# Kernel tuning notes

Hardware: AMD Instinct MI355X
Metric: run time of the kernel (lower is better)

Reference implementation:

```python
import jax, jax.numpy as jnp
import numpy as np

IN, H, T = 512, 1024, 1024


def _xavier(key, shape):
    a = (6.0 / (shape[0] + shape[1])) ** 0.5
    return jax.random.uniform(key, shape, minval=-a, maxval=a, dtype=jnp.float32)


def setup_inputs() -> dict:
    key = jax.random.key(0)
    ks = jax.random.split(key, 20)
    inp = {
        'x': jax.random.normal(ks[0], (1, T, IN), dtype=jnp.float32),
        'time': jax.random.uniform(ks[1], (T,), dtype=jnp.float32),
    }
    # initial states ~ N(0, 0.1) as in the source forward
    names = ['h0_1', 'c0_1', 'h0_2', 'c0_2', 'h0_3', 'c0_3']
    for i, n in enumerate(names):
        inp[n] = 0.1 * jax.random.normal(ks[2 + i], (1, H), dtype=jnp.float32)
    # LSTMCell params: weights xavier_uniform, biases uniform(0,1) (torch gate order i,f,g,o)
    inp['W_ih1'] = _xavier(ks[8], (4 * H, IN + 1))
    inp['W_hh1'] = _xavier(ks[9], (4 * H, H))
    inp['b_ih1'] = jax.random.uniform(ks[10], (4 * H,), dtype=jnp.float32)
    inp['b_hh1'] = jax.random.uniform(ks[11], (4 * H,), dtype=jnp.float32)
    inp['W_ih2'] = _xavier(ks[12], (4 * H, H))
    inp['W_hh2'] = _xavier(ks[13], (4 * H, H))
    inp['b_ih2'] = jax.random.uniform(ks[14], (4 * H,), dtype=jnp.float32)
    inp['b_hh2'] = jax.random.uniform(ks[15], (4 * H,), dtype=jnp.float32)
    return inp


def reference(x, time, h0_1, c0_1, h0_2, c0_2, h0_3, c0_3,
              W_ih1, W_hh1, b_ih1, b_hh1, W_ih2, W_hh2, b_ih2, b_hh2):
    def cell(xt, h, c, W_ih, W_hh, b_ih, b_hh):
        gates = xt @ W_ih.T + b_ih + h @ W_hh.T + b_hh  # (1, 4H)
        i, f, g, o = jnp.split(gates, 4, axis=-1)
        c_new = jax.nn.sigmoid(f) * c + jax.nn.sigmoid(i) * jnp.tanh(g)
        h_new = jax.nn.sigmoid(o) * jnp.tanh(c_new)
        return h_new, c_new

    xs = jnp.concatenate([x[0], time[:, None]], axis=1)  # (T, IN+1)

    def step(carry, xt):
        h1, c1, h2, c2, h3, c3 = carry
        h1, c1 = cell(xt[None, :], h1, c1, W_ih1, W_hh1, b_ih1, b_hh1)
        h2, c2 = cell(h1, h2, c2, W_ih2, W_hh2, b_ih2, b_hh2)
        # source calls self.lstm2 again for the third layer (lstm3 unused)
        h3, c3 = cell(h2, h3, c3, W_ih2, W_hh2, b_ih2, b_hh2)
        return (h1, c1, h2, c2, h3, c3), h3[0]

    carry, hs = jax.lax.scan(step, (h0_1, c0_1, h0_2, c0_2, h0_3, c0_3), xs)
    hs = hs[None]              # (1, T, H)
    h_final = carry[4]         # (1, H) -- last h3
    attn = jnp.einsum('bth,bh->bt', hs, h_final)
    w = jax.nn.softmax(attn, axis=1)
    context = jnp.einsum('bth,bt->bh', hs, w)  # (1, H)
    return context
```

## Files before the change

### kernel.cpp

```cpp
#include <hip/hip_runtime.h>
#include <hip/hip_fp16.h>

#define TSTEPS 1024
#define HDIM   1024
#define INDIM  512
#define NGATE  4096
#define NWG_L1  64
#define NWG_L23 128
#define NWG_TOT 192
#define POISON_U 0x7C7C7C7Cu
#define SPIN_MAX (1 << 20)


typedef _Float16 half2v __attribute__((ext_vector_type(2)));
typedef decltype(__builtin_amdgcn_cvt_pkrtz(0.f, 0.f)) f16x2b;

#define PINU(v) asm volatile("" : "+v"(v))

#if defined(__has_builtin)
#if __has_builtin(__builtin_amdgcn_fdot2)
#define HAVE_FDOT2 1
#endif
#endif

#ifdef HAVE_FDOT2
__device__ __forceinline__ float dot2f(unsigned h, unsigned w, float c) {
    return __builtin_amdgcn_fdot2(__builtin_bit_cast(f16x2b, h),
                                  __builtin_bit_cast(f16x2b, w), c, false);
}
#else
__device__ __forceinline__ float dot2f(unsigned h, unsigned w, float c) {
    half2v a = __builtin_bit_cast(half2v, h);
    half2v b = __builtin_bit_cast(half2v, w);
    c = fmaf((float)a[0], (float)b[0], c);
    c = fmaf((float)a[1], (float)b[1], c);
    return c;
}
#endif

__device__ __forceinline__ float wave_sum64_dpp(float v) {
    int x;
    x = __builtin_amdgcn_update_dpp(0, __float_as_int(v), 0x111, 0xf, 0xf, false); v += __int_as_float(x);
    x = __builtin_amdgcn_update_dpp(0, __float_as_int(v), 0x112, 0xf, 0xf, false); v += __int_as_float(x);
    x = __builtin_amdgcn_update_dpp(0, __float_as_int(v), 0x114, 0xf, 0xf, false); v += __int_as_float(x);
    x = __builtin_amdgcn_update_dpp(0, __float_as_int(v), 0x118, 0xf, 0xf, false); v += __int_as_float(x);
    x = __builtin_amdgcn_update_dpp(0, __float_as_int(v), 0x142, 0xa, 0xf, false); v += __int_as_float(x);
    x = __builtin_amdgcn_update_dpp(0, __float_as_int(v), 0x143, 0xc, 0xf, false); v += __int_as_float(x);
    return v;
}

__device__ __forceinline__ float sigm(float x) { return 1.f / (1.f + __expf(-x)); }
__device__ __forceinline__ float fast_tanh(float x) {
    float t = __expf(-2.f * fabsf(x));
    float r = (1.f - t) / (1.f + t);
    return copysignf(r, x);
}

__device__ __forceinline__ unsigned pack_h(float a, float b) {
    auto p = __builtin_amdgcn_cvt_pkrtz(a, b);
    return __builtin_bit_cast(unsigned, p);
}

__device__ __forceinline__ unsigned agent_loadu(const unsigned* p) {
    return __hip_atomic_load(const_cast<unsigned*>(p), __ATOMIC_RELAXED,
                             __HIP_MEMORY_SCOPE_AGENT);
}
__device__ __forceinline__ void agent_storeu(unsigned* p, unsigned v) {
    __hip_atomic_store(p, v, __ATOMIC_RELAXED, __HIP_MEMORY_SCOPE_AGENT);
}
__device__ __forceinline__ float agent_loadf(const float* p) {
    return __hip_atomic_load(const_cast<float*>(p), __ATOMIC_RELAXED,
                             __HIP_MEMORY_SCOPE_AGENT);
}
__device__ __forceinline__ void agent_storef(float* p, float v) {
    __hip_atomic_store(p, v, __ATOMIC_RELAXED, __HIP_MEMORY_SCOPE_AGENT);
}
__device__ __forceinline__ bool isp(float v) { return __float_as_uint(v) == POISON_U; }

__global__ __launch_bounds__(256) void pack_f16(
    const float* __restrict__ src, unsigned* __restrict__ dst, int n)
{
    int i = blockIdx.x * 256 + threadIdx.x;
    if (i < n) {
        float2 v = *(const float2*)(src + 2 * (size_t)i);
        dst[i] = (unsigned)__half_as_ushort(__float2half(v.x)) |
                 ((unsigned)__half_as_ushort(__float2half(v.y)) << 16);
    }
}

#define BM 64
#define BN 64
#define BK 32
#define GK (INDIM + 1)

__device__ __forceinline__ void gemm_tile(
    int bm, int bn, int ttid,
    const float* __restrict__ B, const float* __restrict__ bias1,
    const float* __restrict__ bias2, float* C,
    const float* __restrict__ x, const float* __restrict__ timev,
    float (*As)[BM + 4], float (*Bs)[BN + 4])
{
    const int t0 = bm * BM;
    const int n0 = bn * BN;
    const int tx = ttid & 15;
    const int ty = ttid >> 4;

    float acc[4][4] = {{0.f}};

    for (int kc = 0; kc < GK; kc += BK) {
#pragma unroll
        for (int i = 0; i < 8; i++) {
            int idx = ttid + i * 256;
            int r = idx >> 5;
            int c = idx & 31;
            int col = kc + c;
            int trow = t0 + r;
            float av = (col < INDIM) ? x[(size_t)trow * INDIM + col]
                                     : ((col == INDIM) ? timev[trow] : 0.f);
            As[c][r] = av;
            int nrow = n0 + r;
            Bs[c][r] = (col < GK) ? B[(size_t)nrow * GK + col] : 0.f;
        }
        __syncthreads();

#pragma unroll
        for (int kk = 0; kk < BK; kk++) {
            float a[4], b[4];
#pragma unroll
            for (int i = 0; i < 4; i++) a[i] = As[kk][ty * 4 + i];
#pragma unroll
            for (int j = 0; j < 4; j++) b[j] = Bs[kk][tx * 4 + j];
#pragma unroll
            for (int i = 0; i < 4; i++)
#pragma unroll
                for (int j = 0; j < 4; j++)
                    acc[i][j] = fmaf(a[i], b[j], acc[i][j]);
        }
        __syncthreads();
    }

#pragma unroll
    for (int i = 0; i < 4; i++) {
        int trow = t0 + ty * 4 + i;
#pragma unroll
        for (int j = 0; j < 4; j++) {
            int n = n0 + tx * 4 + j;
            agent_storef(C + (size_t)trow * NGATE + n,
                         acc[i][j] + bias1[n] + bias2[n]);
        }
    }
}

__global__ __launch_bounds__(1024, 4) void fused_scan(
    const unsigned* __restrict__ Wp1,
    float* G1,
    const unsigned* __restrict__ Wpi2,
    const unsigned* __restrict__ Wph2,
    const float* __restrict__ Wih1,
    const float* __restrict__ bih1, const float* __restrict__ bhh1,
    const float* __restrict__ xin, const float* __restrict__ timev,
    const float* bih2, const float* bhh2,
    const float* h0_1, const float* c0_1,
    const float* h0_2, const float* c0_2,
    const float* h0_3, const float* c0_3,
    unsigned* H1p, unsigned* H2p, unsigned* H3p,
    float* H3f)
{
    __shared__ unsigned shp1[512];
    __shared__ unsigned shp2[512];
    __shared__ unsigned shp3[512];
    __shared__ float gbuf[16][4];
    __shared__ float AsT[4][BK][BM + 4];
    __shared__ float BsT[4][BK][BN + 4];

    const int tid = threadIdx.x;
    const int wg  = blockIdx.x;
    const int q   = tid >> 6;
    const int s   = tid & 63;

    if (wg < NWG_L1) {
        const int u0 = wg << 4;
        const int u  = u0 + q;
        unsigned w[4][8];
#pragma unroll
        for (int g = 0; g < 4; ++g) {
            const unsigned* row = Wp1 + (size_t)((g << 10) + u) * 512 + s;
#pragma unroll
            for (int m = 0; m < 8; ++m)
                w[g][m] = row[64 * m];
        }
        float c1 = (tid < 16) ? c0_1[u0 + tid] : 0.f;
        unsigned pv = 0u;

        for (int t = 0; t < TSTEPS; ++t) {
#pragma unroll
            for (int g = 0; g < 4; ++g)
#pragma unroll
                for (int m = 0; m < 8; ++m) PINU(w[g][m]);

            float Gv0 = 0.f, Gv1 = 0.f, Gv2 = 0.f, Gv3 = 0.f;
            if (tid < 16) {
                const float* gptr = G1 + (size_t)t * NGATE + u0 + tid;
                Gv0 = agent_loadf(gptr);
                Gv1 = agent_loadf(gptr + 1024);
                Gv2 = agent_loadf(gptr + 2048);
                Gv3 = agent_loadf(gptr + 3072);
            }
            if (tid < 512) {
                if (t == 0) {
                    shp1[tid] = pack_h(h0_1[2 * tid], h0_1[2 * tid + 1]);
                } else {
                    const unsigned* p = H1p + (size_t)(t - 1) * 512 + tid;
                    unsigned v = pv;
                    for (int it = 0; it < SPIN_MAX; ++it) {
                        if (__ballot(v == POISON_U) == 0ULL) break;
                        __builtin_amdgcn_s_sleep(1);
                        if (v == POISON_U) v = agent_loadu(p);
                    }
                    shp1[tid] = v;
                }
            }
            __syncthreads();

            float a0 = 0.f, a1 = 0.f, a2 = 0.f, a3 = 0.f;
#pragma unroll
            for (int m = 0; m < 8; ++m) {
                unsigned hu = shp1[s + 64 * m];
                a0 = dot2f(hu, w[0][m], a0);
                a1 = dot2f(hu, w[1][m], a1);
                a2 = dot2f(hu, w[2][m], a2);
                a3 = dot2f(hu, w[3][m], a3);
            }
            a0 = wave_sum64_dpp(a0);
            a1 = wave_sum64_dpp(a1);
            a2 = wave_sum64_dpp(a2);
            a3 = wave_sum64_dpp(a3);
            if (s == 63) {
                gbuf[q][0] = a0;
                gbuf[q][1] = a1;
                gbuf[q][2] = a2;
                gbuf[q][3] = a3;
            }
            __syncthreads();

            if (tid < 16) {
                const float* gptr = G1 + (size_t)t * NGATE + u0 + tid;
                for (int it = 0; it < SPIN_MAX; ++it) {
                    if (__ballot(isp(Gv0) | isp(Gv1) | isp(Gv2) | isp(Gv3)) == 0ULL)
                        break;
                    __builtin_amdgcn_s_sleep(1);
                    if (isp(Gv0)) Gv0 = agent_loadf(gptr);
                    if (isp(Gv1)) Gv1 = agent_loadf(gptr + 1024);
                    if (isp(Gv2)) Gv2 = agent_loadf(gptr + 2048);
                    if (isp(Gv3)) Gv3 = agent_loadf(gptr + 3072);
                }
                float gi = gbuf[tid][0] + Gv0;
                float gf = gbuf[tid][1] + Gv1;
                float gg = gbuf[tid][2] + Gv2;
                float go = gbuf[tid][3] + Gv3;
                float i_ = sigm(gi), f_ = sigm(gf), g_ = fast_tanh(gg), o_ = sigm(go);
                c1 = f_ * c1 + i_ * g_;
                float hn = o_ * fast_tanh(c1);
                float hnn = __shfl_down(hn, 1, 64);
                if (!(tid & 1))
                    agent_storeu(H1p + (size_t)t * 512 + (u0 >> 1) + (tid >> 1),
                                 pack_h(hn, hnn));
            }
            if (tid < 512 && t < TSTEPS - 1) {
                pv = agent_loadu(H1p + (size_t)t * 512 + tid);
                PINU(pv);
            }
        }
    } else {
        {
            const int team = tid >> 8;
            const int ttid = tid & 255;
            const int tg   = (wg - NWG_L1) * 4 + team;
#pragma unroll
            for (int r = 0; r < 2; ++r) {
                const int wk = tg + r * 512;
                gemm_tile(wk >> 6, wk & 63, ttid, Wih1, bih1, bhh1, G1,
                          xin, timev, AsT[team], BsT[team]);
            }
        }
        __syncthreads();

        const int ul = q >> 1;
        const int gp = q & 1;
        const int u0 = (wg - NWG_L1) << 3;
        const int u  = u0 + ul;
        unsigned wi[2][8], wh[2][8];
#pragma unroll
        for (int j = 0; j < 2; ++j) {
            const unsigned* ri = Wpi2 + (size_t)(((2 * gp + j) << 10) + u) * 512 + s;
            const unsigned* rh = Wph2 + (size_t)(((2 * gp + j) << 10) + u) * 512 + s;
#pragma unroll
            for (int m = 0; m < 8; ++m) {
                wi[j][m] = ri[64 * m];
                wh[j][m] = rh[64 * m];
            }
        }
        float bias0 = 0.f, bias1v = 0.f, bias2v = 0.f, bias3 = 0.f, cst = 0.f;
        if (tid < 16) {
            int uu = u0 + (tid & 7);
            bias0  = bih2[uu]        + bhh2[uu];
            bias1v = bih2[1024 + uu] + bhh2[1024 + uu];
            bias2v = bih2[2048 + uu] + bhh2[2048 + uu];
            bias3  = bih2[3072 + uu] + bhh2[3072 + uu];
            cst = (tid < 8) ? c0_2[u0 + tid] : c0_3[u0 + tid - 8];
        }
        unsigned pv1 = 0u;
        if (tid < 512) pv1 = agent_loadu(H1p + tid);

        for (int t = 0; t <= TSTEPS; ++t) {
#pragma unroll
            for (int j = 0; j < 2; ++j)
#pragma unroll
                for (int m = 0; m < 8; ++m) { PINU(wi[j][m]); PINU(wh[j][m]); }

            const bool do2 = (t < TSTEPS);
            const bool do3 = (t >= 1);

            if (tid < 512 && do2) {
                const unsigned* p = H1p + (size_t)t * 512 + tid;
                unsigned v = pv1;
                for (int it = 0; it < SPIN_MAX; ++it) {
                    if (__ballot(v == POISON_U) == 0ULL) break;
                    __builtin_amdgcn_s_sleep(1);
                    if (v == POISON_U) v = agent_loadu(p);
                }
                shp1[tid] = v;
            }
            __syncthreads();

            float p20 = 0.f, p21 = 0.f;
#pragma unroll
            for (int m = 0; m < 8; ++m) {
                unsigned h1u = shp1[s + 64 * m];
                p20 = dot2f(h1u, wi[0][m], p20);
                p21 = dot2f(h1u, wi[1][m], p21);
            }

            if (tid < 512) {
                if (t == 0) {
                    shp2[tid] = pack_h(h0_2[2 * tid], h0_2[2 * tid + 1]);
                } else {
                    const unsigned* p = H2p + (size_t)(t - 1) * 512 + tid;
                    unsigned v = agent_loadu(p);
                    for (int it = 0; it < SPIN_MAX; ++it) {
                        if (__ballot(v == POISON_U) == 0ULL) break;
                        __builtin_amdgcn_s_sleep(1);
                        if (v == POISON_U) v = agent_loadu(p);
                    }
                    shp2[tid] = v;
                }
            } else {
                const int sid = tid - 512;
                if (t == 1) {
                    shp3[sid] = pack_h(h0_3[2 * sid], h0_3[2 * sid + 1]);
                } else if (t > 1) {
                    const unsigned* p = H3p + (size_t)(t - 2) * 512 + sid;
                    unsigned v = agent_loadu(p);
                    for (int it = 0; it < SPIN_MAX; ++it) {
                        if (__ballot(v == POISON_U) == 0ULL) break;
                        __builtin_amdgcn_s_sleep(1);
                        if (v == POISON_U) v = agent_loadu(p);
                    }
                    shp3[sid] = v;
                }
            }
            __syncthreads();

            float p30 = 0.f, p31 = 0.f;
#pragma unroll
            for (int m = 0; m < 8; ++m) {
                unsigned h2u = shp2[s + 64 * m];
                unsigned h3u = shp3[s + 64 * m];
                p20 = dot2f(h2u, wh[0][m], p20);
                p21 = dot2f(h2u, wh[1][m], p21);
                p30 = dot2f(h2u, wi[0][m], p30);
                p31 = dot2f(h2u, wi[1][m], p31);
                p30 = dot2f(h3u, wh[0][m], p30);
                p31 = dot2f(h3u, wh[1][m], p31);
            }
            float s20 = wave_sum64_dpp(p20);
            float s21 = wave_sum64_dpp(p21);
            float s30 = wave_sum64_dpp(p30);
            float s31 = wave_sum64_dpp(p31);
            if (s == 63) {
                gbuf[ul][2 * gp]          = s20;
                gbuf[ul][2 * gp + 1]      = s21;
                gbuf[8 + ul][2 * gp]      = s30;
                gbuf[8 + ul][2 * gp + 1]  = s31;
            }
            __syncthreads();

            if (tid < 16) {
                const bool act = (tid < 8) ? do2 : do3;
                float hn = 0.f;
                if (act) {
                    float gi = gbuf[tid][0] + bias0;
                    float gf = gbuf[tid][1] + bias1v;
                    float gg = gbuf[tid][2] + bias2v;
                    float go = gbuf[tid][3] + bias3;
                    float i_ = sigm(gi), f_ = sigm(gf), g_ = fast_tanh(gg), o_ = sigm(go);
                    cst = f_ * cst + i_ * g_;
                    hn = o_ * fast_tanh(cst);
                }
                float hnn = __shfl_down(hn, 1, 64);
                if (act) {
                    if (tid < 8) {
                        if (!(tid & 1))
                            agent_storeu(H2p + (size_t)t * 512 + (u0 >> 1) + (tid >> 1),
                                         pack_h(hn, hnn));
                    } else {
                        if (!(tid & 1))
                            agent_storeu(H3p + (size_t)(t - 1) * 512 + (u0 >> 1) + ((tid - 8) >> 1),
                                         pack_h(hn, hnn));
                        H3f[(size_t)(t - 1) * HDIM + u0 + (tid - 8)] = hn;
                    }
                }
            }
            if (tid < 512 && t < TSTEPS - 1) {
                pv1 = agent_loadu(H1p + (size_t)(t + 1) * 512 + tid);
                PINU(pv1);
            }
        }
    }
}

__global__ __launch_bounds__(256) void attn_dot(
    const float* __restrict__ H3, float* __restrict__ attn)
{
    const int t = blockIdx.x * 4 + (threadIdx.x >> 6);
    const int lane = threadIdx.x & 63;
    const float* hrow = H3 + (size_t)t * HDIM;
    const float* hf = H3 + (size_t)(TSTEPS - 1) * HDIM;
    float p = 0.f;
    for (int j = lane; j < HDIM; j += 64) p = fmaf(hrow[j], hf[j], p);
#pragma unroll
    for (int d = 32; d; d >>= 1) p += __shfl_down(p, d, 64);
    if (lane == 0) attn[t] = p;
}

__global__ __launch_bounds__(64) void softmax_1024(float* attn)
{
    const int lane = threadIdx.x;
    float vals[16];
    float m = -1e30f;
#pragma unroll
    for (int i = 0; i < 16; i++) {
        vals[i] = attn[lane + i * 64];
        m = fmaxf(m, vals[i]);
    }
#pragma unroll
    for (int d = 32; d; d >>= 1) m = fmaxf(m, __shfl_xor(m, d, 64));
    float s = 0.f;
#pragma unroll
    for (int i = 0; i < 16; i++) {
        vals[i] = expf(vals[i] - m);
        s += vals[i];
    }
#pragma unroll
    for (int d = 32; d; d >>= 1) s += __shfl_xor(s, d, 64);
    float inv = 1.f / s;
#pragma unroll
    for (int i = 0; i < 16; i++) attn[lane + i * 64] = vals[i] * inv;
}

__global__ __launch_bounds__(256) void context_kernel(
    const float* __restrict__ H3, const float* __restrict__ w,
    float* __restrict__ out)
{
    const int u = blockIdx.x * 4 + (threadIdx.x >> 6);
    const int lane = threadIdx.x & 63;
    float p = 0.f;
    for (int t = lane; t < TSTEPS; t += 64)
        p = fmaf(H3[(size_t)t * HDIM + u], w[t], p);
#pragma unroll
    for (int d = 32; d; d >>= 1) p += __shfl_down(p, d, 64);
    if (lane == 0) out[u] = p;
}

extern "C" void kernel_launch(void* const* d_in, const int* in_sizes, int n_in,
                              void* d_out, int out_size, void* d_ws, size_t ws_size,
                              hipStream_t stream)
{
    const float* x     = (const float*)d_in[0];
    const float* timev = (const float*)d_in[1];
    const float* h0_1  = (const float*)d_in[2];
    const float* c0_1  = (const float*)d_in[3];
    const float* h0_2  = (const float*)d_in[4];
    const float* c0_2  = (const float*)d_in[5];
    const float* h0_3  = (const float*)d_in[6];
    const float* c0_3  = (const float*)d_in[7];
    const float* Wih1  = (const float*)d_in[8];
    const float* Whh1  = (const float*)d_in[9];
    const float* bih1  = (const float*)d_in[10];
    const float* bhh1  = (const float*)d_in[11];
    const float* Wih2  = (const float*)d_in[12];
    const float* Whh2  = (const float*)d_in[13];
    const float* bih2  = (const float*)d_in[14];
    const float* bhh2  = (const float*)d_in[15];

    float* G      = (float*)d_ws;
    unsigned* H1p = (unsigned*)(G + (size_t)TSTEPS * NGATE);
    unsigned* H2p = H1p + (size_t)TSTEPS * 512;
    unsigned* H3p = H2p + (size_t)TSTEPS * 512;
    float* H3f    = (float*)(H3p + (size_t)TSTEPS * 512);
    float* attn   = H3f + (size_t)TSTEPS * HDIM;
    unsigned* Wp1  = (unsigned*)(attn + 1024);
    unsigned* Wpi2 = Wp1 + (size_t)NGATE * 512;
    unsigned* Wph2 = Wpi2 + (size_t)NGATE * 512;
    float* out  = (float*)d_out;

    hipMemsetAsync(G, 0x7C,
                   (size_t)TSTEPS * NGATE * sizeof(float) +
                   (size_t)3 * TSTEPS * 512 * sizeof(unsigned), stream);

    {
        const int n = NGATE * 512;
        pack_f16<<<dim3(n / 256), dim3(256), 0, stream>>>(Whh1, Wp1, n);
        pack_f16<<<dim3(n / 256), dim3(256), 0, stream>>>(Wih2, Wpi2, n);
        pack_f16<<<dim3(n / 256), dim3(256), 0, stream>>>(Whh2, Wph2, n);
    }

    {
        const unsigned* a0 = Wp1;  float* a1 = G;
        const unsigned* a2 = Wpi2; const unsigned* a3 = Wph2;
        const float* a4 = Wih1;  const float* a5 = bih1;  const float* a6 = bhh1;
        const float* a7 = x;     const float* a8 = timev;
        const float* a9 = bih2;  const float* a10 = bhh2;
        const float* a11 = h0_1; const float* a12 = c0_1;
        const float* a13 = h0_2; const float* a14 = c0_2;
        const float* a15 = h0_3; const float* a16 = c0_3;
        unsigned* a17 = H1p; unsigned* a18 = H2p; unsigned* a19 = H3p;
        float* a20 = H3f;
        void* args[] = {&a0,&a1,&a2,&a3,&a4,&a5,&a6,&a7,&a8,&a9,&a10,&a11,
                        &a12,&a13,&a14,&a15,&a16,&a17,&a18,&a19,&a20};
        hipLaunchCooperativeKernel((void*)fused_scan, dim3(NWG_TOT), dim3(1024),
                                   args, 0, stream);
    }

    attn_dot<<<dim3(256), dim3(256), 0, stream>>>(H3f, attn);
    softmax_1024<<<dim3(1), dim3(64), 0, stream>>>(attn);
    context_kernel<<<dim3(256), dim3(256), 0, stream>>>(H3f, attn, out);
}
```

Before: 2.784 ms.

## Fuse weight packing and attention epilogue into the cooperative scan kernel

Removes the three separate fp16 packing kernels. Each workgroup now converts its fp32 weight rows to packed half2 in registers at load time. The attention dot, softmax and context kernels are folded into the end of the cooperative kernel and separated by grid-wide atomic barriers. This cuts several kernel launches and the workspace round trip of the packed weights, at the cost of spin barriers and a single-workgroup softmax. Shared-memory tile padding also changes from +4 to +1.

```diff
diff --git a/kernel.cpp b/kernel.cpp
--- a/kernel.cpp
+++ b/kernel.cpp
@@ -77,15 +77,18 @@
 }
 __device__ __forceinline__ bool isp(float v) { return __float_as_uint(v) == POISON_U; }
 
-__global__ __launch_bounds__(256) void pack_f16(
-    const float* __restrict__ src, unsigned* __restrict__ dst, int n)
-{
-    int i = blockIdx.x * 256 + threadIdx.x;
-    if (i < n) {
-        float2 v = *(const float2*)(src + 2 * (size_t)i);
-        dst[i] = (unsigned)__half_as_ushort(__float2half(v.x)) |
-                 ((unsigned)__half_as_ushort(__float2half(v.y)) << 16);
-    }
+__device__ __forceinline__ void grid_barrier(int* bar, int idx, int tid) {
+    __syncthreads();
+    if (tid == 0) {
+        __hip_atomic_fetch_add(&bar[idx], 1, __ATOMIC_ACQ_REL,
+                               __HIP_MEMORY_SCOPE_AGENT);
+        for (int it = 0; it < SPIN_MAX; ++it) {
+            if (__hip_atomic_load(&bar[idx], __ATOMIC_ACQUIRE,
+                                  __HIP_MEMORY_SCOPE_AGENT) >= NWG_TOT) break;
+            __builtin_amdgcn_s_sleep(2);
+        }
+    }
+    __syncthreads();
 }
 
 #define BM 64
@@ -98,7 +101,7 @@
     const float* __restrict__ B, const float* __restrict__ bias1,
     const float* __restrict__ bias2, float* C,
     const float* __restrict__ x, const float* __restrict__ timev,
-    float (*As)[BM + 4], float (*Bs)[BN + 4])
+    float (*As)[BM + 1], float (*Bs)[BN + 1])
 {
     const int t0 = bm * BM;
     const int n0 = bn * BN;
@@ -152,10 +155,10 @@
 }
 
 __global__ __launch_bounds__(1024, 4) void fused_scan(
-    const unsigned* __restrict__ Wp1,
+    const float* __restrict__ Whh1,
     float* G1,
-    const unsigned* __restrict__ Wpi2,
-    const unsigned* __restrict__ Wph2,
+    const float* __restrict__ Wih2,
+    const float* __restrict__ Whh2,
     const float* __restrict__ Wih1,
     const float* __restrict__ bih1, const float* __restrict__ bhh1,
     const float* __restrict__ xin, const float* __restrict__ timev,
@@ -164,14 +167,15 @@
     const float* h0_2, const float* c0_2,
     const float* h0_3, const float* c0_3,
     unsigned* H1p, unsigned* H2p, unsigned* H3p,
-    float* H3f)
+    float* H3f,
+    float* attnb, float* outp, int* bar)
 {
     __shared__ unsigned shp1[512];
     __shared__ unsigned shp2[512];
     __shared__ unsigned shp3[512];
     __shared__ float gbuf[16][4];
-    __shared__ float AsT[4][BK][BM + 4];
-    __shared__ float BsT[4][BK][BN + 4];
+    __shared__ float AsT[4][BK][BM + 1];
+    __shared__ float BsT[4][BK][BN + 1];
 
     const int tid = threadIdx.x;
     const int wg  = blockIdx.x;
@@ -184,10 +188,12 @@
         unsigned w[4][8];
 #pragma unroll
         for (int g = 0; g < 4; ++g) {
-            const unsigned* row = Wp1 + (size_t)((g << 10) + u) * 512 + s;
-#pragma unroll
-            for (int m = 0; m < 8; ++m)
-                w[g][m] = row[64 * m];
+            const float* row = Whh1 + (size_t)((g << 10) + u) * 1024 + 2 * s;
+#pragma unroll
+            for (int m = 0; m < 8; ++m) {
+                float2 v = *(const float2*)(row + 128 * m);
+                w[g][m] = pack_h(v.x, v.y);
+            }
         }
         float c1 = (tid < 16) ? c0_1[u0 + tid] : 0.f;
         unsigned pv = 0u;
@@ -292,12 +298,14 @@
         unsigned wi[2][8], wh[2][8];
 #pragma unroll
         for (int j = 0; j < 2; ++j) {
-            const unsigned* ri = Wpi2 + (size_t)(((2 * gp + j) << 10) + u) * 512 + s;
-            const unsigned* rh = Wph2 + (size_t)(((2 * gp + j) << 10) + u) * 512 + s;
+            const float* ri = Wih2 + (size_t)(((2 * gp + j) << 10) + u) * 1024 + 2 * s;
+            const float* rh = Whh2 + (size_t)(((2 * gp + j) << 10) + u) * 1024 + 2 * s;
 #pragma unroll
             for (int m = 0; m < 8; ++m) {
-                wi[j][m] = ri[64 * m];
-                wh[j][m] = rh[64 * m];
+                float2 vi = *(const float2*)(ri + 128 * m);
+                float2 vh = *(const float2*)(rh + 128 * m);
+                wi[j][m] = pack_h(vi.x, vi.y);
+                wh[j][m] = pack_h(vh.x, vh.y);
             }
         }
         float bias0 = 0.f, bias1v = 0.f, bias2v = 0.f, bias3 = 0.f, cst = 0.f;
@@ -417,7 +425,7 @@
                         if (!(tid & 1))
                             agent_storeu(H3p + (size_t)(t - 1) * 512 + (u0 >> 1) + ((tid - 8) >> 1),
                                          pack_h(hn, hnn));
-                        H3f[(size_t)(t - 1) * HDIM + u0 + (tid - 8)] = hn;
+                        agent_storef(H3f + (size_t)(t - 1) * HDIM + u0 + (tid - 8), hn);
                     }
                 }
             }
@@ -427,59 +435,55 @@
             }
         }
     }
-}
-
-__global__ __launch_bounds__(256) void attn_dot(
-    const float* __restrict__ H3, float* __restrict__ attn)
-{
-    const int t = blockIdx.x * 4 + (threadIdx.x >> 6);
-    const int lane = threadIdx.x & 63;
-    const float* hrow = H3 + (size_t)t * HDIM;
-    const float* hf = H3 + (size_t)(TSTEPS - 1) * HDIM;
-    float p = 0.f;
-    for (int j = lane; j < HDIM; j += 64) p = fmaf(hrow[j], hf[j], p);
-#pragma unroll
-    for (int d = 32; d; d >>= 1) p += __shfl_down(p, d, 64);
-    if (lane == 0) attn[t] = p;
-}
-
-__global__ __launch_bounds__(64) void softmax_1024(float* attn)
-{
-    const int lane = threadIdx.x;
-    float vals[16];
-    float m = -1e30f;
-#pragma unroll
-    for (int i = 0; i < 16; i++) {
-        vals[i] = attn[lane + i * 64];
-        m = fmaxf(m, vals[i]);
-    }
-#pragma unroll
-    for (int d = 32; d; d >>= 1) m = fmaxf(m, __shfl_xor(m, d, 64));
-    float s = 0.f;
-#pragma unroll
-    for (int i = 0; i < 16; i++) {
-        vals[i] = expf(vals[i] - m);
-        s += vals[i];
-    }
-#pragma unroll
-    for (int d = 32; d; d >>= 1) s += __shfl_xor(s, d, 64);
-    float inv = 1.f / s;
-#pragma unroll
-    for (int i = 0; i < 16; i++) attn[lane + i * 64] = vals[i] * inv;
-}
-
-__global__ __launch_bounds__(256) void context_kernel(
-    const float* __restrict__ H3, const float* __restrict__ w,
-    float* __restrict__ out)
-{
-    const int u = blockIdx.x * 4 + (threadIdx.x >> 6);
-    const int lane = threadIdx.x & 63;
-    float p = 0.f;
-    for (int t = lane; t < TSTEPS; t += 64)
-        p = fmaf(H3[(size_t)t * HDIM + u], w[t], p);
-#pragma unroll
-    for (int d = 32; d; d >>= 1) p += __shfl_down(p, d, 64);
-    if (lane == 0) out[u] = p;
+
+    const int gw = wg * 16 + q;
+    grid_barrier(bar, 0, tid);
+
+    if (gw < TSTEPS) {
+        const float* hrow = H3f + (size_t)gw * HDIM;
+        const float* hf   = H3f + (size_t)(TSTEPS - 1) * HDIM;
+        float p = 0.f;
+#pragma unroll
+        for (int j = 0; j < 16; ++j) {
+            int k = s + 64 * j;
+            p = fmaf(agent_loadf(hrow + k), agent_loadf(hf + k), p);
+        }
+        p = wave_sum64_dpp(p);
+        if (s == 63) agent_storef(attnb + gw, p);
+    }
+    grid_barrier(bar, 1, tid);
+
+    if (wg == 0 && tid < 64) {
+        float m = -1e30f;
+        for (int i = 0; i < 16; ++i)
+            m = fmaxf(m, agent_loadf(attnb + tid + i * 64));
+#pragma unroll
+        for (int d = 32; d; d >>= 1) m = fmaxf(m, __shfl_xor(m, d, 64));
+        float ss = 0.f;
+        for (int i = 0; i < 16; ++i)
+            ss += __expf(agent_loadf(attnb + tid + i * 64) - m);
+#pragma unroll
+        for (int d = 32; d; d >>= 1) ss += __shfl_xor(ss, d, 64);
+        float inv = 1.f / ss;
+        for (int i = 0; i < 16; ++i) {
+            int idx = tid + i * 64;
+            agent_storef(attnb + idx,
+                         __expf(agent_loadf(attnb + idx) - m) * inv);
+        }
+    }
+    grid_barrier(bar, 2, tid);
+
+    if (gw < HDIM) {
+        float p = 0.f;
+#pragma unroll
+        for (int j = 0; j < 16; ++j) {
+            int t = s + 64 * j;
+            p = fmaf(agent_loadf(H3f + (size_t)t * HDIM + gw),
+                     agent_loadf(attnb + t), p);
+        }
+        p = wave_sum64_dpp(p);
+        if (s == 63) outp[gw] = p;
+    }
 }
 
 extern "C" void kernel_launch(void* const* d_in, const int* in_sizes, int n_in,
@@ -508,26 +512,18 @@
     unsigned* H2p = H1p + (size_t)TSTEPS * 512;
     unsigned* H3p = H2p + (size_t)TSTEPS * 512;
     float* H3f    = (float*)(H3p + (size_t)TSTEPS * 512);
-    float* attn   = H3f + (size_t)TSTEPS * HDIM;
-    unsigned* Wp1  = (unsigned*)(attn + 1024);
-    unsigned* Wpi2 = Wp1 + (size_t)NGATE * 512;
-    unsigned* Wph2 = Wpi2 + (size_t)NGATE * 512;
-    float* out  = (float*)d_out;
+    float* attnb  = H3f + (size_t)TSTEPS * HDIM;
+    int* bar      = (int*)(attnb + 1024);
+    float* out    = (float*)d_out;
 
     hipMemsetAsync(G, 0x7C,
                    (size_t)TSTEPS * NGATE * sizeof(float) +
                    (size_t)3 * TSTEPS * 512 * sizeof(unsigned), stream);
+    hipMemsetAsync(bar, 0, 16 * sizeof(int), stream);
 
     {
-        const int n = NGATE * 512;
-        pack_f16<<<dim3(n / 256), dim3(256), 0, stream>>>(Whh1, Wp1, n);
-        pack_f16<<<dim3(n / 256), dim3(256), 0, stream>>>(Wih2, Wpi2, n);
-        pack_f16<<<dim3(n / 256), dim3(256), 0, stream>>>(Whh2, Wph2, n);
-    }
-
-    {
-        const unsigned* a0 = Wp1;  float* a1 = G;
-        const unsigned* a2 = Wpi2; const unsigned* a3 = Wph2;
+        const float* a0 = Whh1;  float* a1 = G;
+        const float* a2 = Wih2;  const float* a3 = Whh2;
         const float* a4 = Wih1;  const float* a5 = bih1;  const float* a6 = bhh1;
         const float* a7 = x;     const float* a8 = timev;
         const float* a9 = bih2;  const float* a10 = bhh2;
@@ -535,14 +531,11 @@
         const float* a13 = h0_2; const float* a14 = c0_2;
         const float* a15 = h0_3; const float* a16 = c0_3;
         unsigned* a17 = H1p; unsigned* a18 = H2p; unsigned* a19 = H3p;
-        float* a20 = H3f;
+        float* a20 = H3f; float* a21 = attnb; float* a22 = out; int* a23 = bar;
         void* args[] = {&a0,&a1,&a2,&a3,&a4,&a5,&a6,&a7,&a8,&a9,&a10,&a11,
-                        &a12,&a13,&a14,&a15,&a16,&a17,&a18,&a19,&a20};
+                        &a12,&a13,&a14,&a15,&a16,&a17,&a18,&a19,&a20,&a21,
+                        &a22,&a23};
         hipLaunchCooperativeKernel((void*)fused_scan, dim3(NWG_TOT), dim3(1024),
                                    args, 0, stream);
     }
-
-    attn_dot<<<dim3(256), dim3(256), 0, stream>>>(H3f, attn);
-    softmax_1024<<<dim3(1), dim3(64), 0, stream>>>(attn);
-    context_kernel<<<dim3(256), dim3(256), 0, stream>>>(H3f, attn, out);
-}
+}
```

Result: slower. 2.892 ms (+3.9%).
